# Performance work log

Hardware: AMD Instinct MI355X
Metric: run time of the kernel (lower is better)

## Reference

```python
import jax, jax.numpy as jnp
import numpy as np

B, N, F_IN, F_OUT = 8, 2048, 64, 64
ALPHA = 0.2  # LeakyReLU negative slope


def setup_inputs() -> dict:
    key = jax.random.key(0)
    k_in, k_adj, k_w, k_a1, k_a2 = jax.random.split(key, 5)
    inp = jax.random.normal(k_in, (B, N, F_IN), dtype=jnp.float32)
    adj = (jax.random.uniform(k_adj, (B, N, N)) < 0.05).astype(jnp.float32)
    # xavier_uniform with gain=sqrt(2)
    def xavier(k, shape):
        fan_in, fan_out = shape[0], shape[1]
        bound = np.sqrt(2.0) * np.sqrt(6.0 / (fan_in + fan_out))
        return jax.random.uniform(k, shape, jnp.float32, -bound, bound)
    W = xavier(k_w, (F_IN, F_OUT))
    a1 = xavier(k_a1, (F_OUT, 1))
    a2 = xavier(k_a2, (F_OUT, 1))
    bias = jnp.full((N, F_OUT), 0.1, dtype=jnp.float32)
    return {"input": inp, "adj": adj, "W": W, "a1": a1, "a2": a2, "bias": bias}


def reference(input, adj, W, a1, a2, bias):
    # h: [B, N, F_OUT]
    h = jnp.einsum("bnf,fo->bno", input, W)
    f1 = h @ a1          # [B, N, 1]
    f2 = h @ a2          # [B, N, 1]
    e = jax.nn.leaky_relu(f1 + jnp.swapaxes(f2, 1, 2), negative_slope=ALPHA)  # [B, N, N]
    # NOTE: original multiplies adj elementwise (not -inf mask) and softmaxes over dim=1
    attention = jax.nn.softmax(adj * e, axis=1)
    h_prime = jnp.einsum("bij,bjo->bio", attention, h) + bias  # bias broadcasts over batch
    h_prime = h_prime + input  # in_features == out_features, no downsample
    return jax.nn.elu(h_prime)
```

## Files before the change

kernel.cpp:

```cpp
#include <hip/hip_runtime.h>
#include <cstdint>
#include <cstddef>

#define Bn 8
#define Nn 2048
#define Fn 64
#define ALPHA 0.2f

__device__ __forceinline__ float lrelu(float x) { return fmaxf(x, ALPHA * x); }

__global__ __launch_bounds__(256) void k1_h_f(
        const float* __restrict__ inp, const float* __restrict__ W,
        const float* __restrict__ a1, const float* __restrict__ a2,
        float* __restrict__ h, float* __restrict__ f1, float* __restrict__ f2) {
    __shared__ float Wl[Fn * Fn];
    __shared__ float inr[4 * Fn];
    int t = threadIdx.x;
    for (int k = t; k < Fn * Fn; k += 256) Wl[k] = W[k];
    size_t row0 = (size_t)blockIdx.x * 4;
    inr[t] = inp[row0 * Fn + t];
    __syncthreads();
    int r = t >> 6, o = t & 63;
    const float* irow = &inr[r * Fn];
    float acc = 0.f;
#pragma unroll
    for (int f = 0; f < Fn; ++f) acc = fmaf(irow[f], Wl[f * Fn + o], acc);
    size_t row = row0 + r;
    h[row * Fn + o] = acc;
    float p = acc * a1[o];
    float q = acc * a2[o];
#pragma unroll
    for (int off = 32; off > 0; off >>= 1) {
        p += __shfl_down(p, off, 64);
        q += __shfl_down(q, off, 64);
    }
    if (o == 0) { f1[row] = p; f2[row] = q; }
}

__global__ __launch_bounds__(256) void k1b_max(
        const float* __restrict__ f1, float* __restrict__ f1max) {
    int b = blockIdx.x, t = threadIdx.x;
    float m = -3.4e38f;
    for (int i = t; i < Nn; i += 256) m = fmaxf(m, f1[b * Nn + i]);
#pragma unroll
    for (int off = 32; off > 0; off >>= 1) m = fmaxf(m, __shfl_down(m, off, 64));
    __shared__ float sm[4];
    if ((t & 63) == 0) sm[t >> 6] = m;
    __syncthreads();
    if (t == 0) f1max[b] = fmaxf(fmaxf(sm[0], sm[1]), fmaxf(sm[2], sm[3]));
}

__global__ __launch_bounds__(512) void k2a_pass(
        const float* __restrict__ adj, const float* __restrict__ f1,
        const float* __restrict__ f2, const float* __restrict__ f1max_p,
        float* __restrict__ Dsum, unsigned short* __restrict__ cnt8,
        unsigned* __restrict__ records, int slice) {
    int b = blockIdx.x;
    int cj = blockIdx.y;
    int j0 = cj * 256;
    int i0 = blockIdx.z * 128;
    int w = threadIdx.x >> 6, lane = threadIdx.x & 63;
    float f1max = f1max_p[b];
    float4 f2v = *(const float4*)&f2[b * Nn + j0 + 4 * lane];
    float Mf0 = fmaxf(lrelu(f1max + f2v.x), 0.f);
    float Mf1 = fmaxf(lrelu(f1max + f2v.y), 0.f);
    float Mf2 = fmaxf(lrelu(f1max + f2v.z), 0.f);
    float Mf3 = fmaxf(lrelu(f1max + f2v.w), 0.f);
    float s0 = 0.f, s1 = 0.f, s2 = 0.f, s3 = 0.f;
    const float* abase = adj + ((size_t)b * Nn) * Nn + j0 + 4 * lane;
    const float* f1b = f1 + b * Nn;
    unsigned long long lt = (1ull << lane) - 1ull;
    unsigned jme = (unsigned)(j0 + 4 * lane) << 16;

    for (int g = 0; g < 4; ++g) {
        int r0 = i0 + w + 32 * g;
        float4 av0 = *(const float4*)(abase + (size_t)(r0 +  0) * Nn);
        float4 av1 = *(const float4*)(abase + (size_t)(r0 +  8) * Nn);
        float4 av2 = *(const float4*)(abase + (size_t)(r0 + 16) * Nn);
        float4 av3 = *(const float4*)(abase + (size_t)(r0 + 24) * Nn);
        float fi0 = f1b[r0], fi1 = f1b[r0 + 8], fi2 = f1b[r0 + 16], fi3 = f1b[r0 + 24];
#define PROC(AV, FI, IROW)                                                       \
        {                                                                        \
            bool n0 = AV.x != 0.f, n1 = AV.y != 0.f,                             \
                 n2 = AV.z != 0.f, n3 = AV.w != 0.f;                             \
            float e0 = __expf((n0 ? lrelu((FI) + f2v.x) : 0.f) - Mf0);           \
            float e1 = __expf((n1 ? lrelu((FI) + f2v.y) : 0.f) - Mf1);           \
            float e2 = __expf((n2 ? lrelu((FI) + f2v.z) : 0.f) - Mf2);           \
            float e3 = __expf((n3 ? lrelu((FI) + f2v.w) : 0.f) - Mf3);           \
            s0 += e0; s1 += e1; s2 += e2; s3 += e3;                              \
            unsigned long long m0 = __ballot(n0), m1 = __ballot(n1),             \
                               m2 = __ballot(n2), m3 = __ballot(n3);             \
            int c0 = __popcll(m0), c1 = __popcll(m1),                            \
                c2 = __popcll(m2), c3 = __popcll(m3);                            \
            int tot = c0 + c1 + c2 + c3;                                         \
            if (tot) {                                                           \
                unsigned* rl = records +                                         \
                    (size_t)(((b * Nn + (IROW)) << 3) + cj) * slice;             \
                int p0 = __popcll(m0 & lt);                                      \
                int p1 = c0 + __popcll(m1 & lt);                                 \
                int p2 = c0 + c1 + __popcll(m2 & lt);                            \
                int p3 = c0 + c1 + c2 + __popcll(m3 & lt);                       \
                if (n0 && p0 < slice)                                            \
                    rl[p0] = (jme + 0x00000) | (__float_as_uint(e0) >> 16);      \
                if (n1 && p1 < slice)                                            \
                    rl[p1] = (jme + 0x10000) | (__float_as_uint(e1) >> 16);      \
                if (n2 && p2 < slice)                                            \
                    rl[p2] = (jme + 0x20000) | (__float_as_uint(e2) >> 16);      \
                if (n3 && p3 < slice)                                            \
                    rl[p3] = (jme + 0x30000) | (__float_as_uint(e3) >> 16);      \
            }                                                                    \
            if (lane == 0)                                                       \
                cnt8[((b * Nn + (IROW)) << 3) + cj] =                            \
                    (unsigned short)(tot < slice ? tot : slice);                 \
        }
        PROC(av0, fi0, r0 +  0)
        PROC(av1, fi1, r0 +  8)
        PROC(av2, fi2, r0 + 16)
        PROC(av3, fi3, r0 + 24)
#undef PROC
    }
    __shared__ float sred[8][256];
    sred[w][4 * lane + 0] = s0;
    sred[w][4 * lane + 1] = s1;
    sred[w][4 * lane + 2] = s2;
    sred[w][4 * lane + 3] = s3;
    __syncthreads();
    if (threadIdx.x < 256) {
        int c = threadIdx.x;
        float v = 0.f;
#pragma unroll
        for (int k = 0; k < 8; ++k) v += sred[k][c];
        atomicAdd(&Dsum[b * Nn + j0 + c], v);
    }
}

__global__ __launch_bounds__(256) void k2b_finalize(
        const float* __restrict__ Dsum, const float* __restrict__ f2,
        const float* __restrict__ f1max_p, const float* __restrict__ h,
        float2* __restrict__ cs, float* __restrict__ hz) {
    int b = blockIdx.x;
    int jbase = blockIdx.y * 128;
    int t = threadIdx.x;
    float f1max = f1max_p[b];
    __shared__ float zsh[128];
    if (t < 128) {
        int j = jbase + t;
        float f2j = f2[b * Nn + j];
        float Mf = fmaxf(lrelu(f1max + f2j), 0.f);
        float R = 1.f / Dsum[b * Nn + j];
        float z = __expf(-Mf) * R;
        cs[b * Nn + j] = make_float2(R, z);
        zsh[t] = z;
    }
    __syncthreads();
    int w = t >> 6, lane = t & 63;
    float acc = 0.f;
#pragma unroll 4
    for (int jj = w; jj < 128; jj += 4)
        acc = fmaf(zsh[jj], h[((size_t)(b * Nn + jbase + jj)) * Fn + lane], acc);
    __shared__ float hred[4][64];
    hred[w][lane] = acc;
    __syncthreads();
    if (w == 0) {
        float v = hred[0][lane] + hred[1][lane] + hred[2][lane] + hred[3][lane];
        atomicAdd(&hz[b * Fn + lane], v);
    }
}

__global__ __launch_bounds__(256) void k3_aggregate(
        const unsigned* __restrict__ records,
        const unsigned short* __restrict__ cnt8,
        const float2* __restrict__ cs,
        const float* __restrict__ h, const float* __restrict__ hz,
        const float* __restrict__ inp, const float* __restrict__ bias,
        float* __restrict__ out, int slice) {
    int b = blockIdx.x;
    int w = threadIdx.x >> 6, lane = threadIdx.x & 63;
    int i = blockIdx.y * 4 + w;
    int row = b * Nn + i;
    const float2* csb = cs + (size_t)b * Nn;
    const float* hb = h + (size_t)b * Nn * Fn;
    const unsigned* rb = records + (size_t)(row << 3) * slice;

    uint4 cw = *(const uint4*)(cnt8 + (row << 3));
    int nc[8] = { (int)(cw.x & 0xffff), (int)(cw.x >> 16),
                  (int)(cw.y & 0xffff), (int)(cw.y >> 16),
                  (int)(cw.z & 0xffff), (int)(cw.z >> 16),
                  (int)(cw.w & 0xffff), (int)(cw.w >> 16) };

    unsigned recs[8];
#pragma unroll
    for (int cj = 0; cj < 8; ++cj) recs[cj] = rb[slice * cj + lane];

    int idxs[8];
    float coefs[8];
#pragma unroll
    for (int cj = 0; cj < 8; ++cj) {
        idxs[cj] = (int)((recs[cj] >> 16) & 2047);
        float val = __uint_as_float(recs[cj] << 16);
        float2 rz = csb[idxs[cj]];
        coefs[cj] = fmaf(val, rz.x, -rz.y);
    }

    float acc = hz[b * Fn + lane];
#pragma unroll
    for (int cj = 0; cj < 8; ++cj) {
        int n = nc[cj];
        for (int k = 0; k < n; ++k) {
            float c = __shfl(coefs[cj], k, 64);
            int j = __shfl(idxs[cj], k, 64);
            acc = fmaf(c, hb[(size_t)j * Fn + lane], acc);
        }
    }
    size_t idxo = (size_t)row * Fn + lane;
    float hp = acc + bias[i * Fn + lane] + inp[idxo];
    out[idxo] = hp > 0.f ? hp : __expf(hp) - 1.f;
}

extern "C" void kernel_launch(void* const* d_in, const int* in_sizes, int n_in,
                              void* d_out, int out_size, void* d_ws, size_t ws_size,
                              hipStream_t stream) {
    const float* inp  = (const float*)d_in[0];
    const float* adj  = (const float*)d_in[1];
    const float* W    = (const float*)d_in[2];
    const float* a1   = (const float*)d_in[3];
    const float* a2   = (const float*)d_in[4];
    const float* bias = (const float*)d_in[5];
    float* out = (float*)d_out;

    float* h      = (float*)d_ws;
    float2* cs    = (float2*)(h + (size_t)Bn * Nn * Fn);
    float* f1     = (float*)(cs + (size_t)Bn * Nn);
    float* f2     = f1 + (size_t)Bn * Nn;
    float* hz     = f2 + (size_t)Bn * Nn;
    float* Dsum   = hz + (size_t)Bn * Fn;
    float* f1max  = Dsum + (size_t)Bn * Nn;
    unsigned short* cnt8 = (unsigned short*)(f1max + 16);
    unsigned* records = (unsigned*)(cnt8 + (size_t)Bn * Nn * 8);

    size_t fixed = (size_t)((char*)records - (char*)d_ws) + 512;
    size_t cap = (ws_size > fixed) ? (ws_size - fixed) / ((size_t)Bn * Nn * 8 * 4) : 0;
    int slice = (cap >= 48) ? 48 : (cap >= 32 ? 32 : 24);

    hipMemsetAsync(hz, 0, ((size_t)Bn * Fn + (size_t)Bn * Nn) * sizeof(float), stream);
    k1_h_f<<<Bn * Nn / 4, 256, 0, stream>>>(inp, W, a1, a2, h, f1, f2);
    k1b_max<<<Bn, 256, 0, stream>>>(f1, f1max);
    k2a_pass<<<dim3(Bn, 8, 16), 512, 0, stream>>>(adj, f1, f2, f1max, Dsum, cnt8, records, slice);
    k2b_finalize<<<dim3(Bn, 16), 256, 0, stream>>>(Dsum, f2, f1max, h, cs, hz);
    k3_aggregate<<<dim3(Bn, Nn / 4), 256, 0, stream>>>(records, cnt8, cs, h, hz, inp, bias, out, slice);
}
```

Measured before the change: 298.1 us.

## Replace sparse record aggregation with dense bf16 MFMA GEMM over attention matrix

The sparse record and count scheme is dropped. The first pass now writes the full unnormalized exp matrix P as bf16, and a new kernel builds a transposed h scaled by 1/Dsum in bf16. The aggregation becomes a dense bf16 MFMA GEMM with a fused bias, residual and ELU epilogue. This removes the irregular gather and shuffle work and the slice-capacity truncation, but adds a 64MB bf16 P write and read plus bf16 rounding of the attention weights and h.

Measured after the change: 277.1 us. -7.1%, faster.

```diff
diff --git a/kernel.cpp b/kernel.cpp
--- a/kernel.cpp
+++ b/kernel.cpp
@@ -7,7 +7,16 @@
 #define Fn 64
 #define ALPHA 0.2f
 
+typedef __attribute__((ext_vector_type(8))) short  s8frag;
+typedef __attribute__((ext_vector_type(4))) float  f4frag;
+
 __device__ __forceinline__ float lrelu(float x) { return fmaxf(x, ALPHA * x); }
+__device__ __forceinline__ float elu(float x)   { return x > 0.f ? x : __expf(x) - 1.f; }
+__device__ __forceinline__ unsigned short bfr(float f) {
+    unsigned u = __float_as_uint(f);
+    u += 0x7fffu + ((u >> 16) & 1u);
+    return (unsigned short)(u >> 16);
+}
 
 __global__ __launch_bounds__(256) void k1_h_f(
         const float* __restrict__ inp, const float* __restrict__ W,
@@ -50,14 +59,12 @@
     if (t == 0) f1max[b] = fmaxf(fmaxf(sm[0], sm[1]), fmaxf(sm[2], sm[3]));
 }
 
-__global__ __launch_bounds__(512) void k2a_pass(
+__global__ __launch_bounds__(512) void k2a_dense(
         const float* __restrict__ adj, const float* __restrict__ f1,
         const float* __restrict__ f2, const float* __restrict__ f1max_p,
-        float* __restrict__ Dsum, unsigned short* __restrict__ cnt8,
-        unsigned* __restrict__ records, int slice) {
+        float* __restrict__ Dsum, unsigned short* __restrict__ P) {
     int b = blockIdx.x;
-    int cj = blockIdx.y;
-    int j0 = cj * 256;
+    int j0 = blockIdx.y * 256;
     int i0 = blockIdx.z * 128;
     int w = threadIdx.x >> 6, lane = threadIdx.x & 63;
     float f1max = f1max_p[b];
@@ -68,9 +75,8 @@
     float Mf3 = fmaxf(lrelu(f1max + f2v.w), 0.f);
     float s0 = 0.f, s1 = 0.f, s2 = 0.f, s3 = 0.f;
     const float* abase = adj + ((size_t)b * Nn) * Nn + j0 + 4 * lane;
+    unsigned short* pbase = P + ((size_t)b * Nn) * Nn + j0 + 4 * lane;
     const float* f1b = f1 + b * Nn;
-    unsigned long long lt = (1ull << lane) - 1ull;
-    unsigned jme = (unsigned)(j0 + 4 * lane) << 16;
 
     for (int g = 0; g < 4; ++g) {
         int r0 = i0 + w + 32 * g;
@@ -79,39 +85,17 @@
         float4 av2 = *(const float4*)(abase + (size_t)(r0 + 16) * Nn);
         float4 av3 = *(const float4*)(abase + (size_t)(r0 + 24) * Nn);
         float fi0 = f1b[r0], fi1 = f1b[r0 + 8], fi2 = f1b[r0 + 16], fi3 = f1b[r0 + 24];
-#define PROC(AV, FI, IROW)                                                       \
-        {                                                                        \
-            bool n0 = AV.x != 0.f, n1 = AV.y != 0.f,                             \
-                 n2 = AV.z != 0.f, n3 = AV.w != 0.f;                             \
-            float e0 = __expf((n0 ? lrelu((FI) + f2v.x) : 0.f) - Mf0);           \
-            float e1 = __expf((n1 ? lrelu((FI) + f2v.y) : 0.f) - Mf1);           \
-            float e2 = __expf((n2 ? lrelu((FI) + f2v.z) : 0.f) - Mf2);           \
-            float e3 = __expf((n3 ? lrelu((FI) + f2v.w) : 0.f) - Mf3);           \
-            s0 += e0; s1 += e1; s2 += e2; s3 += e3;                              \
-            unsigned long long m0 = __ballot(n0), m1 = __ballot(n1),             \
-                               m2 = __ballot(n2), m3 = __ballot(n3);             \
-            int c0 = __popcll(m0), c1 = __popcll(m1),                            \
-                c2 = __popcll(m2), c3 = __popcll(m3);                            \
-            int tot = c0 + c1 + c2 + c3;                                         \
-            if (tot) {                                                           \
-                unsigned* rl = records +                                         \
-                    (size_t)(((b * Nn + (IROW)) << 3) + cj) * slice;             \
-                int p0 = __popcll(m0 & lt);                                      \
-                int p1 = c0 + __popcll(m1 & lt);                                 \
-                int p2 = c0 + c1 + __popcll(m2 & lt);                            \
-                int p3 = c0 + c1 + c2 + __popcll(m3 & lt);                       \
-                if (n0 && p0 < slice)                                            \
-                    rl[p0] = (jme + 0x00000) | (__float_as_uint(e0) >> 16);      \
-                if (n1 && p1 < slice)                                            \
-                    rl[p1] = (jme + 0x10000) | (__float_as_uint(e1) >> 16);      \
-                if (n2 && p2 < slice)                                            \
-                    rl[p2] = (jme + 0x20000) | (__float_as_uint(e2) >> 16);      \
-                if (n3 && p3 < slice)                                            \
-                    rl[p3] = (jme + 0x30000) | (__float_as_uint(e3) >> 16);      \
-            }                                                                    \
-            if (lane == 0)                                                       \
-                cnt8[((b * Nn + (IROW)) << 3) + cj] =                            \
-                    (unsigned short)(tot < slice ? tot : slice);                 \
+#define PROC(AV, FI, IROW)                                                     \
+        {                                                                      \
+            float e0 = __expf((AV.x != 0.f ? lrelu((FI) + f2v.x) : 0.f) - Mf0);\
+            float e1 = __expf((AV.y != 0.f ? lrelu((FI) + f2v.y) : 0.f) - Mf1);\
+            float e2 = __expf((AV.z != 0.f ? lrelu((FI) + f2v.z) : 0.f) - Mf2);\
+            float e3 = __expf((AV.w != 0.f ? lrelu((FI) + f2v.w) : 0.f) - Mf3);\
+            s0 += e0; s1 += e1; s2 += e2; s3 += e3;                            \
+            uint2 pk;                                                          \
+            pk.x = (unsigned)bfr(e0) | ((unsigned)bfr(e1) << 16);              \
+            pk.y = (unsigned)bfr(e2) | ((unsigned)bfr(e3) << 16);              \
+            *(uint2*)(pbase + (size_t)(IROW) * Nn) = pk;                       \
         }
         PROC(av0, fi0, r0 +  0)
         PROC(av1, fi1, r0 +  8)
@@ -134,87 +118,84 @@
     }
 }
 
-__global__ __launch_bounds__(256) void k2b_finalize(
-        const float* __restrict__ Dsum, const float* __restrict__ f2,
-        const float* __restrict__ f1max_p, const float* __restrict__ h,
-        float2* __restrict__ cs, float* __restrict__ hz) {
+__global__ __launch_bounds__(256) void k2b_scale_T(
+        const float* __restrict__ h, const float* __restrict__ Dsum,
+        unsigned short* __restrict__ hTs) {
     int b = blockIdx.x;
-    int jbase = blockIdx.y * 128;
+    int j0 = blockIdx.y * 64;
     int t = threadIdx.x;
-    float f1max = f1max_p[b];
-    __shared__ float zsh[128];
-    if (t < 128) {
-        int j = jbase + t;
-        float f2j = f2[b * Nn + j];
-        float Mf = fmaxf(lrelu(f1max + f2j), 0.f);
-        float R = 1.f / Dsum[b * Nn + j];
-        float z = __expf(-Mf) * R;
-        cs[b * Nn + j] = make_float2(R, z);
-        zsh[t] = z;
-    }
-    __syncthreads();
-    int w = t >> 6, lane = t & 63;
-    float acc = 0.f;
-#pragma unroll 4
-    for (int jj = w; jj < 128; jj += 4)
-        acc = fmaf(zsh[jj], h[((size_t)(b * Nn + jbase + jj)) * Fn + lane], acc);
-    __shared__ float hred[4][64];
-    hred[w][lane] = acc;
-    __syncthreads();
-    if (w == 0) {
-        float v = hred[0][lane] + hred[1][lane] + hred[2][lane] + hred[3][lane];
-        atomicAdd(&hz[b * Fn + lane], v);
-    }
-}
-
-__global__ __launch_bounds__(256) void k3_aggregate(
-        const unsigned* __restrict__ records,
-        const unsigned short* __restrict__ cnt8,
-        const float2* __restrict__ cs,
-        const float* __restrict__ h, const float* __restrict__ hz,
+    __shared__ float Lh[64][68];
+    __shared__ float Rsh[64];
+    if (t < 64) Rsh[t] = 1.f / Dsum[b * Nn + j0 + t];
+#pragma unroll
+    for (int q = 0; q < 4; ++q) {
+        int fi = t + 256 * q;
+        int jj = fi >> 4, oq = fi & 15;
+        float4 v = *(const float4*)(h + ((size_t)(b * Nn + j0 + jj)) * Fn + oq * 4);
+        *(float4*)&Lh[jj][oq * 4] = v;
+    }
+    __syncthreads();
+    int o = t >> 2, jg = (t & 3) * 16;
+    unsigned wbuf[8];
+#pragma unroll
+    for (int s2 = 0; s2 < 8; ++s2) {
+        int j = jg + 2 * s2;
+        unsigned lo16 = bfr(Lh[j][o] * Rsh[j]);
+        unsigned hi16 = bfr(Lh[j + 1][o] * Rsh[j + 1]);
+        wbuf[s2] = lo16 | (hi16 << 16);
+    }
+    unsigned short* dst = hTs + ((size_t)(b * Fn + o)) * Nn + j0 + jg;
+    *(uint4*)dst       = make_uint4(wbuf[0], wbuf[1], wbuf[2], wbuf[3]);
+    *(uint4*)(dst + 8) = make_uint4(wbuf[4], wbuf[5], wbuf[6], wbuf[7]);
+}
+
+__global__ __launch_bounds__(256) void k3_gemm(
+        const unsigned short* __restrict__ P, const unsigned short* __restrict__ hTs,
         const float* __restrict__ inp, const float* __restrict__ bias,
-        float* __restrict__ out, int slice) {
+        float* __restrict__ out) {
     int b = blockIdx.x;
     int w = threadIdx.x >> 6, lane = threadIdx.x & 63;
-    int i = blockIdx.y * 4 + w;
-    int row = b * Nn + i;
-    const float2* csb = cs + (size_t)b * Nn;
-    const float* hb = h + (size_t)b * Nn * Fn;
-    const unsigned* rb = records + (size_t)(row << 3) * slice;
-
-    uint4 cw = *(const uint4*)(cnt8 + (row << 3));
-    int nc[8] = { (int)(cw.x & 0xffff), (int)(cw.x >> 16),
-                  (int)(cw.y & 0xffff), (int)(cw.y >> 16),
-                  (int)(cw.z & 0xffff), (int)(cw.z >> 16),
-                  (int)(cw.w & 0xffff), (int)(cw.w >> 16) };
-
-    unsigned recs[8];
-#pragma unroll
-    for (int cj = 0; cj < 8; ++cj) recs[cj] = rb[slice * cj + lane];
-
-    int idxs[8];
-    float coefs[8];
-#pragma unroll
-    for (int cj = 0; cj < 8; ++cj) {
-        idxs[cj] = (int)((recs[cj] >> 16) & 2047);
-        float val = __uint_as_float(recs[cj] << 16);
-        float2 rz = csb[idxs[cj]];
-        coefs[cj] = fmaf(val, rz.x, -rz.y);
-    }
-
-    float acc = hz[b * Fn + lane];
-#pragma unroll
-    for (int cj = 0; cj < 8; ++cj) {
-        int n = nc[cj];
-        for (int k = 0; k < n; ++k) {
-            float c = __shfl(coefs[cj], k, 64);
-            int j = __shfl(idxs[cj], k, 64);
-            acc = fmaf(c, hb[(size_t)j * Fn + lane], acc);
-        }
-    }
-    size_t idxo = (size_t)row * Fn + lane;
-    float hp = acc + bias[i * Fn + lane] + inp[idxo];
-    out[idxo] = hp > 0.f ? hp : __expf(hp) - 1.f;
+    int laneM = lane & 15, laneK = (lane >> 4) * 8;
+    int i0 = blockIdx.y * 32 + (w >> 1) * 16;
+    int o0 = (w & 1) * 32;
+    const unsigned short* A0 = hTs + ((size_t)(b * Fn + o0 + laneM)) * Nn + laneK;
+    const unsigned short* A1 = A0 + 16 * Nn;
+    const unsigned short* Bp = P + ((size_t)(b * Nn + i0 + laneM)) * Nn + laneK;
+
+    f4frag c0 = {0.f, 0.f, 0.f, 0.f}, c1 = {0.f, 0.f, 0.f, 0.f};
+    s8frag a0 = *(const s8frag*)A0;
+    s8frag a1 = *(const s8frag*)A1;
+    s8frag bb = *(const s8frag*)Bp;
+#pragma unroll 4
+    for (int k0 = 32; k0 < Nn; k0 += 32) {
+        s8frag na0 = *(const s8frag*)(A0 + k0);
+        s8frag na1 = *(const s8frag*)(A1 + k0);
+        s8frag nbb = *(const s8frag*)(Bp + k0);
+        c0 = __builtin_amdgcn_mfma_f32_16x16x32_bf16(a0, bb, c0, 0, 0, 0);
+        c1 = __builtin_amdgcn_mfma_f32_16x16x32_bf16(a1, bb, c1, 0, 0, 0);
+        a0 = na0; a1 = na1; bb = nbb;
+    }
+    c0 = __builtin_amdgcn_mfma_f32_16x16x32_bf16(a0, bb, c0, 0, 0, 0);
+    c1 = __builtin_amdgcn_mfma_f32_16x16x32_bf16(a1, bb, c1, 0, 0, 0);
+
+    int i = i0 + laneM;
+    int oA = o0 + (lane >> 4) * 4;
+    size_t gbase = ((size_t)b * Nn + i) * Fn;
+    float4 in0 = *(const float4*)(inp + gbase + oA);
+    float4 in1 = *(const float4*)(inp + gbase + oA + 16);
+    float4 bi0 = *(const float4*)(bias + (size_t)i * Fn + oA);
+    float4 bi1 = *(const float4*)(bias + (size_t)i * Fn + oA + 16);
+    float4 r0v, r1v;
+    r0v.x = elu(c0[0] + in0.x + bi0.x);
+    r0v.y = elu(c0[1] + in0.y + bi0.y);
+    r0v.z = elu(c0[2] + in0.z + bi0.z);
+    r0v.w = elu(c0[3] + in0.w + bi0.w);
+    r1v.x = elu(c1[0] + in1.x + bi1.x);
+    r1v.y = elu(c1[1] + in1.y + bi1.y);
+    r1v.z = elu(c1[2] + in1.z + bi1.z);
+    r1v.w = elu(c1[3] + in1.w + bi1.w);
+    *(float4*)(out + gbase + oA) = r0v;
+    *(float4*)(out + gbase + oA + 16) = r1v;
 }
 
 extern "C" void kernel_launch(void* const* d_in, const int* in_sizes, int n_in,
@@ -228,24 +209,18 @@
     const float* bias = (const float*)d_in[5];
     float* out = (float*)d_out;
 
-    float* h      = (float*)d_ws;
-    float2* cs    = (float2*)(h + (size_t)Bn * Nn * Fn);
-    float* f1     = (float*)(cs + (size_t)Bn * Nn);
-    float* f2     = f1 + (size_t)Bn * Nn;
-    float* hz     = f2 + (size_t)Bn * Nn;
-    float* Dsum   = hz + (size_t)Bn * Fn;
-    float* f1max  = Dsum + (size_t)Bn * Nn;
-    unsigned short* cnt8 = (unsigned short*)(f1max + 16);
-    unsigned* records = (unsigned*)(cnt8 + (size_t)Bn * Nn * 8);
-
-    size_t fixed = (size_t)((char*)records - (char*)d_ws) + 512;
-    size_t cap = (ws_size > fixed) ? (ws_size - fixed) / ((size_t)Bn * Nn * 8 * 4) : 0;
-    int slice = (cap >= 48) ? 48 : (cap >= 32 ? 32 : 24);
-
-    hipMemsetAsync(hz, 0, ((size_t)Bn * Fn + (size_t)Bn * Nn) * sizeof(float), stream);
+    unsigned short* P   = (unsigned short*)d_ws;
+    unsigned short* hTs = P + (size_t)Bn * Nn * Nn;
+    float* h     = (float*)(hTs + (size_t)Bn * Fn * Nn);
+    float* f1    = h + (size_t)Bn * Nn * Fn;
+    float* f2    = f1 + (size_t)Bn * Nn;
+    float* Dsum  = f2 + (size_t)Bn * Nn;
+    float* f1max = Dsum + (size_t)Bn * Nn;
+
+    hipMemsetAsync(Dsum, 0, (size_t)Bn * Nn * sizeof(float), stream);
     k1_h_f<<<Bn * Nn / 4, 256, 0, stream>>>(inp, W, a1, a2, h, f1, f2);
     k1b_max<<<Bn, 256, 0, stream>>>(f1, f1max);
-    k2a_pass<<<dim3(Bn, 8, 16), 512, 0, stream>>>(adj, f1, f2, f1max, Dsum, cnt8, records, slice);
-    k2b_finalize<<<dim3(Bn, 16), 256, 0, stream>>>(Dsum, f2, f1max, h, cs, hz);
-    k3_aggregate<<<dim3(Bn, Nn / 4), 256, 0, stream>>>(records, cnt8, cs, h, hz, inp, bias, out, slice);
-}
+    k2a_dense<<<dim3(Bn, Nn / 256, Nn / 128), 512, 0, stream>>>(adj, f1, f2, f1max, Dsum, P);
+    k2b_scale_T<<<dim3(Bn, Nn / 64), 256, 0, stream>>>(h, Dsum, hTs);
+    k3_gemm<<<dim3(Bn, Nn / 32), 256, 0, stream>>>(P, hTs, inp, bias, out);
+}
```
